# Kernel optimization log

Measured on AMD Instinct MI355X. Metric: run time of the kernel, lower is better.

## Reference

```python
import jax, jax.numpy as jnp
import numpy as np

NUM_HEADS = 16
DIM_HEAD = 64
DIM = 1024
SCALE = DIM ** (-0.5)  # NOTE: source scales by model dim, not dim_head


def setup_inputs() -> dict:
    key = jax.random.key(0)
    ks = jax.random.split(key, 6)
    b, n, d = 2, 2048, DIM
    return {
        "x": jax.random.normal(ks[0], (b, n, d), dtype=jnp.float32),
        "mask": jnp.ones((b, n), dtype=bool),
        "Wq": jax.random.normal(ks[1], (NUM_HEADS * DIM_HEAD, d), dtype=jnp.float32) * 0.02,
        "Wk": jax.random.normal(ks[2], (DIM_HEAD, d), dtype=jnp.float32) * 0.02,
        "Wv": jax.random.normal(ks[3], (DIM_HEAD, d), dtype=jnp.float32) * 0.02,
        "Wfc": jax.random.normal(ks[4], (d, NUM_HEADS * DIM_HEAD), dtype=jnp.float32) * 0.02,
        "bfc": jnp.zeros((d,), dtype=jnp.float32),
    }


def reference(x, mask, Wq, Wk, Wv, Wfc, bfc):
    b, n, _ = x.shape
    # projections (nn.Linear: y = x @ W.T)
    q = (x @ Wq.T).reshape(b, n, NUM_HEADS, DIM_HEAD).transpose(0, 2, 1, 3)  # b h n d
    k = x @ Wk.T  # b n d  (single shared MQA head)
    v = x @ Wv.T  # b n d
    energy = jnp.einsum("bhid,bjd->bhij", q, k) * SCALE  # b h i j
    mask_value = -jnp.finfo(energy.dtype).max
    # input mask: k_mask is all ones in source, so only query rows are masked
    q_mask = mask[:, None, :, None]  # b 1 i 1
    energy = jnp.where(q_mask, energy, mask_value)
    # causal mask: positions j > i are masked (i == j since self-attention)
    i = jnp.arange(n)
    causal = i[:, None] < i[None, :]  # True where future
    energy = jnp.where(causal[None, None, :, :], mask_value, energy)
    attn = jax.nn.softmax(energy, axis=-1)
    # dropout_rate = 0.0 -> identity
    out = jnp.einsum("bhij,bjd->bhid", attn, v)
    out = out.transpose(0, 2, 1, 3).reshape(b, n, NUM_HEADS * DIM_HEAD)
    return out @ Wfc.T + bfc
```

## Files before the change

kernel.cpp:

```cpp
#include <hip/hip_runtime.h>
#include <math.h>

#define NH 16
#define DH 64
#define DM 1024
#define NS 2048
#define BB 2
#define MR (BB * NS)
#define LDQ 1152
#define C_EXP 0.0450842201f

typedef unsigned short u16;
typedef __attribute__((ext_vector_type(8))) short short8;
typedef __attribute__((ext_vector_type(4))) short short4v;
typedef __attribute__((ext_vector_type(4))) float floatx4;
typedef __attribute__((ext_vector_type(4))) u16 u16x4;

#if __has_builtin(__builtin_amdgcn_exp2f)
#define EXP2(x) __builtin_amdgcn_exp2f(x)
#else
#define EXP2(x) exp2f(x)
#endif

#define MFMA16(a, b, c) __builtin_amdgcn_mfma_f32_16x16x32_bf16((a), (b), (c), 0, 0, 0)

#if __has_builtin(__builtin_amdgcn_mfma_f32_16x16x16bf16_1k)
#define MFMAK16(a, b, c) __builtin_amdgcn_mfma_f32_16x16x16bf16_1k((a), (b), (c), 0, 0, 0)
#else
static __device__ __forceinline__ floatx4 mfmak16_(short4v a, short4v b, floatx4 c) {
  asm("v_mfma_f32_16x16x16_bf16 %0, %1, %2, %0" : "+v"(c) : "v"(a), "v"(b));
  return c;
}
#define MFMAK16(a, b, c) mfmak16_((a), (b), (c))
#endif

static __device__ __forceinline__ u16 f2bf(float f) {
  union { float f; unsigned u; } v; v.f = f;
  unsigned r = v.u + 0x7fffu + ((v.u >> 16) & 1u);
  return (u16)(r >> 16);
}
static __device__ __forceinline__ u16 f2bf_fast(float f) {
  union { float f; unsigned u; } v; v.f = f;
  return (u16)((v.u + 0x8000u) >> 16);
}

#define GLDS16(gp, lp)                                                        \
  __builtin_amdgcn_global_load_lds(                                           \
      (const __attribute__((address_space(1))) void*)(const void*)(gp),       \
      (__attribute__((address_space(3))) void*)(void*)(lp), 16, 0, 0)

__global__ __launch_bounds__(256) void cast_all(
    const float* __restrict__ x, const float* __restrict__ wq,
    const float* __restrict__ wk, const float* __restrict__ wv,
    const float* __restrict__ wfc, u16* __restrict__ xb,
    u16* __restrict__ wqkvb, u16* __restrict__ wfcb) {
  const int NX = MR * DM / 4, NQ = DM * DM / 4, NK = DH * DM / 4;
  int id = blockIdx.x * 256 + threadIdx.x;
  const float* src;
  u16* dst;
  int off;
  if (id < NX) { src = x; dst = xb; off = id; }
  else if (id < NX + NQ) { src = wq; dst = wqkvb; off = id - NX; }
  else if (id < NX + NQ + NK) { src = wk; dst = wqkvb + (size_t)DM * DM; off = id - NX - NQ; }
  else if (id < NX + NQ + 2 * NK) { src = wv; dst = wqkvb + (size_t)(DM + DH) * DM; off = id - NX - NQ - NK; }
  else { src = wfc; dst = wfcb; off = id - NX - NQ - 2 * NK; }
  float4 f = ((const float4*)src)[off];
  u16x4 o;
  o[0] = f2bf(f.x); o[1] = f2bf(f.y); o[2] = f2bf(f.z); o[3] = f2bf(f.w);
  ((u16x4*)dst)[off] = o;
}

__global__ __launch_bounds__(256) void gemm64(
    const u16* __restrict__ A, const u16* __restrict__ W,
    const float* __restrict__ bias, void* __restrict__ Cout,
    u16* __restrict__ vT, int M, int N, int K, int ldc, int out_bf16,
    int v_by) {
  __shared__ u16 As[2][64 * 32];
  __shared__ u16 Ws[2][64 * 32];
  const int tid = threadIdx.x;
  const int lane = tid & 63;
  const int lr = lane & 15, quad = lane >> 4;
  const int wave = tid >> 6, wr = wave >> 1, wc = wave & 1;

  const int lin = blockIdx.y * gridDim.x + blockIdx.x;
  const int xcd = lin & 7, slot = lin >> 3;
  const int bx = xcd * 8 + (slot & 7), by = slot >> 3;
  const int m0 = bx * 64, n0 = by * 64;

  const int srow = tid >> 2;
  const int scg = (tid & 3) ^ ((srow >> 1) & 3);
  const u16* gA = A + (size_t)(m0 + srow) * K + scg * 8;
  const u16* gW = W + (size_t)(n0 + srow) * K + scg * 8;
  const int lo = wave * 512;

  floatx4 acc[2][2] = {};
  const int nt = K >> 5;

  GLDS16(gA, &As[0][lo]);
  GLDS16(gW, &Ws[0][lo]);

  for (int t = 0; t < nt; ++t) {
    __syncthreads();
    if (t + 1 < nt) {
      const int ko = (t + 1) << 5;
      const int nb = (t + 1) & 1;
      GLDS16(gA + ko, &As[nb][lo]);
      GLDS16(gW + ko, &Ws[nb][lo]);
    }
    const u16* as = As[t & 1];
    const u16* ws = Ws[t & 1];
    short8 af[2], wf[2];
#pragma unroll
    for (int mi = 0; mi < 2; ++mi) {
      int rr = wr * 32 + mi * 16 + lr;
      af[mi] = *(const short8*)&as[rr * 32 + ((quad ^ ((rr >> 1) & 3)) << 3)];
    }
#pragma unroll
    for (int nj = 0; nj < 2; ++nj) {
      int rc = wc * 32 + nj * 16 + lr;
      wf[nj] = *(const short8*)&ws[rc * 32 + ((quad ^ ((rc >> 1) & 3)) << 3)];
    }
#pragma unroll
    for (int mi = 0; mi < 2; ++mi)
#pragma unroll
      for (int nj = 0; nj < 2; ++nj)
        acc[mi][nj] = MFMA16(af[mi], wf[nj], acc[mi][nj]);
  }

  if (v_by >= 0 && by == v_by) {
#pragma unroll
    for (int mi = 0; mi < 2; ++mi)
#pragma unroll
      for (int nj = 0; nj < 2; ++nj)
#pragma unroll
        for (int r = 0; r < 4; ++r)
          vT[(size_t)(wc * 32 + nj * 16 + lr) * MR + m0 + wr * 32 + mi * 16 +
             quad * 4 + r] = f2bf(acc[mi][nj][r]);
    return;
  }

#pragma unroll
  for (int mi = 0; mi < 2; ++mi) {
#pragma unroll
    for (int nj = 0; nj < 2; ++nj) {
      int col = n0 + wc * 32 + nj * 16 + lr;
      float badd = bias ? bias[col] : 0.f;
#pragma unroll
      for (int r = 0; r < 4; ++r) {
        int row = m0 + wr * 32 + mi * 16 + quad * 4 + r;
        float v = acc[mi][nj][r] + badd;
        if (out_bf16)
          ((u16*)Cout)[(size_t)row * ldc + col] = f2bf(v);
        else
          ((float*)Cout)[(size_t)row * ldc + col] = v;
      }
    }
  }
}

__global__ __launch_bounds__(512) void attn_mfma(
    const u16* __restrict__ qkv,
    const u16* __restrict__ vT,
    u16* __restrict__ aob) {
  __shared__ __align__(16) u16 smem[4 * 8192];

  const int b = blockIdx.z;
  const int p = blockIdx.x;
  const int tid = threadIdx.x;
  const int lane = tid & 63;
  const int lr = lane & 15, quad = lane >> 4;
  const int w = tid >> 6;
  const int hl = w & 3;
  const int half = w >> 2;
  const int head = blockIdx.y * 4 + hl;
  const int hb = half * 64;
  const size_t rowb = (size_t)b * NS;
  const u16* kvK = qkv + rowb * LDQ + 1024;
  const u16* vTb = vT + rowb;

  int skrow[2], skcg[2], svrow[2], svcg[2], lo[2];
#pragma unroll
  for (int g = 0; g < 2; ++g) {
    const int ci = g * 512 + tid;
    skrow[g] = ci >> 3;
    skcg[g] = (ci & 7) ^ (skrow[g] & 7);
    svrow[g] = ci >> 4;
    svcg[g] = (ci & 15) ^ (svrow[g] & 15);
    lo[g] = (g * 512 + w * 64) * 8;
  }

  for (int phase = 0; phase < 2; ++phase) {
    const int s = (phase == 0) ? (63 - p) : p;
    const int i0q = s * 32;
    const int ntp = (s >> 2) + 1;
    const int irowA = i0q + lr;
    const int irowB = i0q + 16 + lr;

    const u16* qpA = qkv + (rowb + i0q + lr) * LDQ + head * DH;
    const u16* qpB = qpA + 16 * LDQ;
    short8 aqA0 = *(const short8*)(qpA + quad * 8);
    short8 aqA1 = *(const short8*)(qpA + 32 + quad * 8);
    short8 aqB0 = *(const short8*)(qpB + quad * 8);
    short8 aqB1 = *(const short8*)(qpB + 32 + quad * 8);

    floatx4 oA[4] = {}, oB[4] = {};
    float laccA = 0.f, laccB = 0.f;

    __syncthreads();
#pragma unroll
    for (int g = 0; g < 2; ++g) {
      GLDS16(kvK + (size_t)skrow[g] * LDQ + skcg[g] * 8, &smem[lo[g]]);
      GLDS16(vTb + (size_t)svrow[g] * MR + svcg[g] * 8, &smem[16384 + lo[g]]);
    }

    for (int t = 0; t < ntp; ++t) {
      const int buf = t & 1;
      __syncthreads();

      if (t + 1 < ntp) {
        const int j0n = (t + 1) * 128;
        const int nb2 = (buf ^ 1) * 8192;
#pragma unroll
        for (int g = 0; g < 2; ++g) {
          GLDS16(kvK + (size_t)(j0n + skrow[g]) * LDQ + skcg[g] * 8,
                 &smem[nb2 + lo[g]]);
          GLDS16(vTb + (size_t)svrow[g] * MR + j0n + svcg[g] * 8,
                 &smem[16384 + nb2 + lo[g]]);
        }
      }

      const int j0 = t * 128;
      const u16* ksb = smem + buf * 8192;
      const u16* vtb = smem + 16384 + buf * 8192;
      const bool lastt = (t == ntp - 1);

      if (lastt && half == 1 && (s & 3) < 2) continue;

#pragma unroll
      for (int jb = 0; jb < 4; ++jb) {
        const int krow = hb + jb * 16 + lr;
        short8 bk0 = *(const short8*)&ksb[krow * 64 + ((quad ^ (krow & 7)) << 3)];
        short8 bk1 = *(const short8*)&ksb[krow * 64 + (((4 + quad) ^ (krow & 7)) << 3)];
        floatx4 zA = {}, zB = {};
        zA = MFMA16(bk0, aqA0, zA);
        zA = MFMA16(bk1, aqA1, zA);
        zB = MFMA16(bk0, aqB0, zB);
        zB = MFMA16(bk1, aqB1, zB);

        const int kbase = j0 + hb + jb * 16 + (quad << 2);
        short4v apA, apB;
#pragma unroll
        for (int r = 0; r < 4; ++r) {
          float peA = EXP2(zA[r] * C_EXP);
          float peB = EXP2(zB[r] * C_EXP);
          if (lastt && (kbase + r > irowA)) peA = 0.f;
          if (lastt && (kbase + r > irowB)) peB = 0.f;
          laccA += peA;
          laccB += peB;
          apA[r] = (short)f2bf_fast(peA);
          apB[r] = (short)f2bf_fast(peB);
        }

#pragma unroll
        for (int nb = 0; nb < 4; ++nb) {
          const int d = nb * 16 + lr;
          const int va = d * 128 +
                         (((8 * half + 2 * jb + (quad >> 1)) ^ (d & 15)) << 3) +
                         ((quad & 1) << 2);
          short4v bv = *(const short4v*)&vtb[va];
          oA[nb] = MFMAK16(apA, bv, oA[nb]);
          oB[nb] = MFMAK16(apB, bv, oB[nb]);
        }
      }
    }

    laccA += __shfl_xor(laccA, 16);
    laccA += __shfl_xor(laccA, 32);
    laccB += __shfl_xor(laccB, 16);
    laccB += __shfl_xor(laccB, 32);

    __syncthreads();
    float* M = (float*)smem;
    float* Mh = M + hl * 34 * 64;
    if (half == 1) {
#pragma unroll
      for (int nb = 0; nb < 4; ++nb)
#pragma unroll
        for (int r = 0; r < 4; ++r) {
          Mh[(nb * 4 + r) * 64 + lane] = oA[nb][r];
          Mh[(16 + nb * 4 + r) * 64 + lane] = oB[nb][r];
        }
      Mh[32 * 64 + lane] = laccA;
      Mh[33 * 64 + lane] = laccB;
    }
    __syncthreads();
    if (half == 0) {
#pragma unroll
      for (int nb = 0; nb < 4; ++nb)
#pragma unroll
        for (int r = 0; r < 4; ++r) {
          oA[nb][r] += Mh[(nb * 4 + r) * 64 + lane];
          oB[nb][r] += Mh[(16 + nb * 4 + r) * 64 + lane];
        }
      laccA += Mh[32 * 64 + lane];
      laccB += Mh[33 * 64 + lane];

      float dA[4], dB[4];
#pragma unroll
      for (int r = 0; r < 4; ++r) {
        dA[r] = __shfl(laccA, (quad << 2) + r);
        dB[r] = __shfl(laccB, (quad << 2) + r);
      }
#pragma unroll
      for (int nb = 0; nb < 4; ++nb)
#pragma unroll
        for (int r = 0; r < 4; ++r) {
          const int col = head * DH + nb * 16 + lr;
          aob[(rowb + i0q + (quad << 2) + r) * DM + col] =
              f2bf(oA[nb][r] / dA[r]);
          aob[(rowb + i0q + 16 + (quad << 2) + r) * DM + col] =
              f2bf(oB[nb][r] / dB[r]);
        }
    }
  }
}

extern "C" void kernel_launch(void* const* d_in, const int* in_sizes, int n_in,
                              void* d_out, int out_size, void* d_ws, size_t ws_size,
                              hipStream_t stream) {
  const float* x = (const float*)d_in[0];
  const float* Wq = (const float*)d_in[2];
  const float* Wk = (const float*)d_in[3];
  const float* Wv = (const float*)d_in[4];
  const float* Wfc = (const float*)d_in[5];
  const float* bfc = (const float*)d_in[6];

  u16* xb = (u16*)d_ws;
  u16* wqkvb = xb + (size_t)MR * DM;
  u16* wfcb = wqkvb + (size_t)LDQ * DM;
  u16* qkv = wfcb + (size_t)DM * DM;
  u16* vT = qkv + (size_t)MR * LDQ;
  u16* aob = xb;

  cast_all<<<dim3((MR * DM + DM * DM * 2 + DH * DM * 2) / 1024), dim3(256), 0,
             stream>>>(x, Wq, Wk, Wv, Wfc, xb, wqkvb, wfcb);
  gemm64<<<dim3(MR / 64, LDQ / 64), dim3(256), 0, stream>>>(
      xb, wqkvb, nullptr, qkv, vT, MR, LDQ, DM, LDQ, 1, 17);
  attn_mfma<<<dim3(32, NH / 4, BB), dim3(512), 0, stream>>>(qkv, vT, aob);
  gemm64<<<dim3(MR / 64, DM / 64), dim3(256), 0, stream>>>(
      aob, wfcb, bfc, d_out, nullptr, MR, DM, DM, DM, 0, -1);
}
```

Baseline: 152.9 us.

## Enlarge projection GEMM tiles to 128x128 with 4x4 MFMA per wave

Replaces the 64x64 GEMM with a 128x128 tile in which each wave computes a 64x64 sub-tile using a 4x4 grid of MFMAs. The shared-memory staging is doubled, with two async loads per thread per operand. The XCD-aware block remapping is dropped, and the V-transpose epilogue is reworked so the wave half covering V columns writes vT while the K half writes normally. The aim is more operand reuse per LDS load and fewer blocks, at the cost of more registers, lower occupancy and roughly one wave of blocks across the CUs.

```diff
diff --git a/kernel.cpp b/kernel.cpp
--- a/kernel.cpp
+++ b/kernel.cpp
@@ -70,84 +70,90 @@
   ((u16x4*)dst)[off] = o;
 }
 
-__global__ __launch_bounds__(256) void gemm64(
+__global__ __launch_bounds__(256) void gemm128(
     const u16* __restrict__ A, const u16* __restrict__ W,
     const float* __restrict__ bias, void* __restrict__ Cout,
-    u16* __restrict__ vT, int M, int N, int K, int ldc, int out_bf16,
-    int v_by) {
-  __shared__ u16 As[2][64 * 32];
-  __shared__ u16 Ws[2][64 * 32];
+    u16* __restrict__ vT, int K, int ldc, int out_bf16, int v_by) {
+  __shared__ u16 As[2][128 * 32];
+  __shared__ u16 Ws[2][128 * 32];
   const int tid = threadIdx.x;
   const int lane = tid & 63;
   const int lr = lane & 15, quad = lane >> 4;
   const int wave = tid >> 6, wr = wave >> 1, wc = wave & 1;
-
-  const int lin = blockIdx.y * gridDim.x + blockIdx.x;
-  const int xcd = lin & 7, slot = lin >> 3;
-  const int bx = xcd * 8 + (slot & 7), by = slot >> 3;
-  const int m0 = bx * 64, n0 = by * 64;
-
-  const int srow = tid >> 2;
-  const int scg = (tid & 3) ^ ((srow >> 1) & 3);
-  const u16* gA = A + (size_t)(m0 + srow) * K + scg * 8;
-  const u16* gW = W + (size_t)(n0 + srow) * K + scg * 8;
-  const int lo = wave * 512;
-
-  floatx4 acc[2][2] = {};
+  const int m0 = blockIdx.x * 128, n0 = blockIdx.y * 128;
+
+  const u16* gA[2];
+  const u16* gW[2];
+  int lbase[2];
+#pragma unroll
+  for (int g = 0; g < 2; ++g) {
+    const int ci = g * 256 + tid;
+    const int row = ci >> 2, slot = ci & 3;
+    const int gch = slot ^ ((row >> 1) & 3);
+    gA[g] = A + (size_t)(m0 + row) * K + gch * 8;
+    gW[g] = W + (size_t)(n0 + row) * K + gch * 8;
+    lbase[g] = (g * 256 + wave * 64) * 8;
+  }
+
+  floatx4 acc[4][4] = {};
   const int nt = K >> 5;
 
-  GLDS16(gA, &As[0][lo]);
-  GLDS16(gW, &Ws[0][lo]);
+  GLDS16(gA[0], &As[0][lbase[0]]);
+  GLDS16(gA[1], &As[0][lbase[1]]);
+  GLDS16(gW[0], &Ws[0][lbase[0]]);
+  GLDS16(gW[1], &Ws[0][lbase[1]]);
 
   for (int t = 0; t < nt; ++t) {
     __syncthreads();
     if (t + 1 < nt) {
       const int ko = (t + 1) << 5;
       const int nb = (t + 1) & 1;
-      GLDS16(gA + ko, &As[nb][lo]);
-      GLDS16(gW + ko, &Ws[nb][lo]);
+      GLDS16(gA[0] + ko, &As[nb][lbase[0]]);
+      GLDS16(gA[1] + ko, &As[nb][lbase[1]]);
+      GLDS16(gW[0] + ko, &Ws[nb][lbase[0]]);
+      GLDS16(gW[1] + ko, &Ws[nb][lbase[1]]);
     }
     const u16* as = As[t & 1];
     const u16* ws = Ws[t & 1];
-    short8 af[2], wf[2];
-#pragma unroll
-    for (int mi = 0; mi < 2; ++mi) {
-      int rr = wr * 32 + mi * 16 + lr;
+    short8 af[4], wf[4];
+#pragma unroll
+    for (int mi = 0; mi < 4; ++mi) {
+      int rr = wr * 64 + mi * 16 + lr;
       af[mi] = *(const short8*)&as[rr * 32 + ((quad ^ ((rr >> 1) & 3)) << 3)];
     }
 #pragma unroll
-    for (int nj = 0; nj < 2; ++nj) {
-      int rc = wc * 32 + nj * 16 + lr;
+    for (int nj = 0; nj < 4; ++nj) {
+      int rc = wc * 64 + nj * 16 + lr;
       wf[nj] = *(const short8*)&ws[rc * 32 + ((quad ^ ((rc >> 1) & 3)) << 3)];
     }
 #pragma unroll
-    for (int mi = 0; mi < 2; ++mi)
-#pragma unroll
-      for (int nj = 0; nj < 2; ++nj)
+    for (int mi = 0; mi < 4; ++mi)
+#pragma unroll
+      for (int nj = 0; nj < 4; ++nj)
         acc[mi][nj] = MFMA16(af[mi], wf[nj], acc[mi][nj]);
   }
 
-  if (v_by >= 0 && by == v_by) {
-#pragma unroll
-    for (int mi = 0; mi < 2; ++mi)
-#pragma unroll
-      for (int nj = 0; nj < 2; ++nj)
+  if (v_by == (int)blockIdx.y && wc == 1) {
+#pragma unroll
+    for (int mi = 0; mi < 4; ++mi)
+#pragma unroll
+      for (int nj = 0; nj < 4; ++nj)
 #pragma unroll
         for (int r = 0; r < 4; ++r)
-          vT[(size_t)(wc * 32 + nj * 16 + lr) * MR + m0 + wr * 32 + mi * 16 +
-             quad * 4 + r] = f2bf(acc[mi][nj][r]);
+          vT[(size_t)(nj * 16 + lr) * MR + m0 + wr * 64 + mi * 16 + quad * 4 +
+             r] = f2bf(acc[mi][nj][r]);
     return;
   }
 
 #pragma unroll
-  for (int mi = 0; mi < 2; ++mi) {
-#pragma unroll
-    for (int nj = 0; nj < 2; ++nj) {
-      int col = n0 + wc * 32 + nj * 16 + lr;
+  for (int mi = 0; mi < 4; ++mi) {
+#pragma unroll
+    for (int nj = 0; nj < 4; ++nj) {
+      int col = n0 + wc * 64 + nj * 16 + lr;
       float badd = bias ? bias[col] : 0.f;
 #pragma unroll
       for (int r = 0; r < 4; ++r) {
-        int row = m0 + wr * 32 + mi * 16 + quad * 4 + r;
+        int row = m0 + wr * 64 + mi * 16 + quad * 4 + r;
         float v = acc[mi][nj][r] + badd;
         if (out_bf16)
           ((u16*)Cout)[(size_t)row * ldc + col] = f2bf(v);
@@ -344,9 +350,9 @@
 
   cast_all<<<dim3((MR * DM + DM * DM * 2 + DH * DM * 2) / 1024), dim3(256), 0,
              stream>>>(x, Wq, Wk, Wv, Wfc, xb, wqkvb, wfcb);
-  gemm64<<<dim3(MR / 64, LDQ / 64), dim3(256), 0, stream>>>(
-      xb, wqkvb, nullptr, qkv, vT, MR, LDQ, DM, LDQ, 1, 17);
+  gemm128<<<dim3(MR / 128, LDQ / 128), dim3(256), 0, stream>>>(
+      xb, wqkvb, nullptr, qkv, vT, DM, LDQ, 1, 8);
   attn_mfma<<<dim3(32, NH / 4, BB), dim3(512), 0, stream>>>(qkv, vT, aob);
-  gemm64<<<dim3(MR / 64, DM / 64), dim3(256), 0, stream>>>(
-      aob, wfcb, bfc, d_out, nullptr, MR, DM, DM, DM, 0, -1);
-}
+  gemm128<<<dim3(MR / 128, DM / 128), dim3(256), 0, stream>>>(
+      aob, wfcb, bfc, d_out, nullptr, DM, DM, 0, -1);
+}
```

Result: slower. 167.3 us (+9.4%).

## Split-K the output projection GEMM into two slices with a reduction kernel

Applied to the files above, without the earlier changes.

The final FC GEMM now runs with a K dimension split into two halves across blockIdx.z, writing fp32 partials to workspace, followed by a new reduce kernel that sums the partials and adds the bias. This doubles the block count to raise parallelism and shorten each block's K loop. The cost is an extra 32 MB of partial writes and reads plus one more kernel launch. The launch bounds also request 8 blocks per CU.

```diff
diff --git a/kernel.cpp b/kernel.cpp
--- a/kernel.cpp
+++ b/kernel.cpp
@@ -70,17 +70,19 @@
   ((u16x4*)dst)[off] = o;
 }
 
-__global__ __launch_bounds__(256) void gemm64(
+__global__ __launch_bounds__(256, 8) void gemm64(
     const u16* __restrict__ A, const u16* __restrict__ W,
     const float* __restrict__ bias, void* __restrict__ Cout,
-    u16* __restrict__ vT, int M, int N, int K, int ldc, int out_bf16,
-    int v_by) {
+    u16* __restrict__ vT, int M, int N, int ldk, int Kc, int ldc,
+    int out_bf16, int v_by) {
   __shared__ u16 As[2][64 * 32];
   __shared__ u16 Ws[2][64 * 32];
   const int tid = threadIdx.x;
   const int lane = tid & 63;
   const int lr = lane & 15, quad = lane >> 4;
   const int wave = tid >> 6, wr = wave >> 1, wc = wave & 1;
+  const int slice = blockIdx.z;
+  const int koff = slice * Kc;
 
   const int lin = blockIdx.y * gridDim.x + blockIdx.x;
   const int xcd = lin & 7, slot = lin >> 3;
@@ -89,12 +91,12 @@
 
   const int srow = tid >> 2;
   const int scg = (tid & 3) ^ ((srow >> 1) & 3);
-  const u16* gA = A + (size_t)(m0 + srow) * K + scg * 8;
-  const u16* gW = W + (size_t)(n0 + srow) * K + scg * 8;
+  const u16* gA = A + (size_t)(m0 + srow) * ldk + koff + scg * 8;
+  const u16* gW = W + (size_t)(n0 + srow) * ldk + koff + scg * 8;
   const int lo = wave * 512;
 
   floatx4 acc[2][2] = {};
-  const int nt = K >> 5;
+  const int nt = Kc >> 5;
 
   GLDS16(gA, &As[0][lo]);
   GLDS16(gW, &Ws[0][lo]);
@@ -139,6 +141,7 @@
     return;
   }
 
+  const size_t sbase = (size_t)slice * M * ldc;
 #pragma unroll
   for (int mi = 0; mi < 2; ++mi) {
 #pragma unroll
@@ -152,10 +155,26 @@
         if (out_bf16)
           ((u16*)Cout)[(size_t)row * ldc + col] = f2bf(v);
         else
-          ((float*)Cout)[(size_t)row * ldc + col] = v;
+          ((float*)Cout)[sbase + (size_t)row * ldc + col] = v;
       }
     }
   }
+}
+
+__global__ __launch_bounds__(256) void reduce_fc(
+    const float4* __restrict__ p, const float4* __restrict__ bias,
+    float4* __restrict__ out) {
+  const size_t NEL = (size_t)MR * DM / 4;
+  size_t i = (size_t)blockIdx.x * 256 + threadIdx.x;
+  float4 a = p[i];
+  float4 b = p[i + NEL];
+  float4 bb = bias[i & (DM / 4 - 1)];
+  float4 o;
+  o.x = a.x + b.x + bb.x;
+  o.y = a.y + b.y + bb.y;
+  o.z = a.z + b.z + bb.z;
+  o.w = a.w + b.w + bb.w;
+  out[i] = o;
 }
 
 __global__ __launch_bounds__(512) void attn_mfma(
@@ -340,13 +359,16 @@
   u16* wfcb = wqkvb + (size_t)LDQ * DM;
   u16* qkv = wfcb + (size_t)DM * DM;
   u16* vT = qkv + (size_t)MR * LDQ;
+  float* pFC = (float*)(vT + (size_t)DH * MR);
   u16* aob = xb;
 
   cast_all<<<dim3((MR * DM + DM * DM * 2 + DH * DM * 2) / 1024), dim3(256), 0,
              stream>>>(x, Wq, Wk, Wv, Wfc, xb, wqkvb, wfcb);
   gemm64<<<dim3(MR / 64, LDQ / 64), dim3(256), 0, stream>>>(
-      xb, wqkvb, nullptr, qkv, vT, MR, LDQ, DM, LDQ, 1, 17);
+      xb, wqkvb, nullptr, qkv, vT, MR, LDQ, DM, DM, LDQ, 1, 17);
   attn_mfma<<<dim3(32, NH / 4, BB), dim3(512), 0, stream>>>(qkv, vT, aob);
-  gemm64<<<dim3(MR / 64, DM / 64), dim3(256), 0, stream>>>(
-      aob, wfcb, bfc, d_out, nullptr, MR, DM, DM, DM, 0, -1);
-}
+  gemm64<<<dim3(MR / 64, DM / 64, 2), dim3(256), 0, stream>>>(
+      aob, wfcb, nullptr, pFC, nullptr, MR, DM, DM, DM / 2, DM, 0, -1);
+  reduce_fc<<<dim3(MR * DM / 4 / 256), dim3(256), 0, stream>>>(
+      (const float4*)pFC, (const float4*)bfc, (float4*)d_out);
+}
```

After: 163.2 us. +6.7%, slower.
